# Performance work log

Measured on AMD Instinct MI355X. Metric: run time of the kernel, lower is better.

## Reference

```python
import jax, jax.numpy as jnp
import numpy as np

K = 9          # 3x3 deformable kernel positions
EPS = 1e-5     # BatchNorm eps


def conv3x3(x, w, stride=1):
    # x: [B,C,H,W], w: [O,I,3,3], padding=1
    return jax.lax.conv_general_dilated(
        x, w, (stride, stride), ((1, 1), (1, 1)),
        dimension_numbers=('NCHW', 'OIHW', 'NCHW'))


def _bilinear_sample(img, py, px):
    # img: [C,H,W]; py,px: [K,Ho,Wo] float sample coords (zero outside).
    H, W = img.shape[1], img.shape[2]
    y0 = jnp.floor(py)
    x0 = jnp.floor(px)

    def corner(yc, xc):
        w = (1.0 - jnp.abs(py - yc)) * (1.0 - jnp.abs(px - xc))
        valid = (yc >= 0) & (yc <= H - 1) & (xc >= 0) & (xc <= W - 1)
        yi = jnp.clip(yc, 0, H - 1).astype(jnp.int32)
        xi = jnp.clip(xc, 0, W - 1).astype(jnp.int32)
        v = img[:, yi, xi]                      # [C,K,Ho,Wo]
        return v * (w * valid)[None]

    return (corner(y0, x0) + corner(y0, x0 + 1) +
            corner(y0 + 1, x0) + corner(y0 + 1, x0 + 1))


def deform_conv2d(x, offset, mask, w, stride=1, pad=1):
    # x: [B,Cin,H,W]; offset: [B,2K,Ho,Wo] (y,x interleaved per tap);
    # mask: [B,K,Ho,Wo]; w: [Cout,Cin,3,3]. torchvision DCNv2 semantics.
    B, Cin = x.shape[0], x.shape[1]
    Ho, Wo = offset.shape[2], offset.shape[3]
    Cout = w.shape[0]
    kh, kw = jnp.meshgrid(jnp.arange(3), jnp.arange(3), indexing='ij')
    kh = kh.reshape(K).astype(x.dtype)
    kw = kw.reshape(K).astype(x.dtype)
    base_y = (jnp.arange(Ho) * stride - pad).astype(x.dtype)
    base_x = (jnp.arange(Wo) * stride - pad).astype(x.dtype)
    off = offset.reshape(B, K, 2, Ho, Wo)
    py = base_y[None, None, :, None] + kh[None, :, None, None] + off[:, :, 0]
    px = base_x[None, None, None, :] + kw[None, :, None, None] + off[:, :, 1]
    g = jax.vmap(_bilinear_sample)(x, py, px)     # [B,Cin,K,Ho,Wo]
    g = g * mask[:, None]
    return jnp.einsum('bikhw,oik->bohw', g, w.reshape(Cout, Cin, K))


def batchnorm(x, gamma, beta, mean, var):
    # eval-mode BN over channel dim of [B,C,H,W]
    inv = jax.lax.rsqrt(var + EPS) * gamma
    return x * inv[None, :, None, None] + (beta - mean * inv)[None, :, None, None]


def setup_inputs() -> dict:
    key = jax.random.key(0)
    ks = jax.random.split(key, 20)
    B, Cin, H, W = 16, 64, 64, 64
    C1, C2, NC = 128, 128, 1000
    inp = {
        'x': jax.random.normal(ks[0], (B, Cin, H, W), jnp.float32),
        'conv1_w': jax.random.normal(ks[1], (C1, Cin, 3, 3), jnp.float32) * 0.05,
        'off1_w': jax.random.normal(ks[2], (2 * K, Cin, 3, 3), jnp.float32) * 0.02,
        'mod1_w': jax.random.normal(ks[3], (K, Cin, 3, 3), jnp.float32) * 0.05,
        'bn1_g': jax.random.uniform(ks[4], (C1,), jnp.float32, 0.5, 1.5),
        'bn1_b': jax.random.normal(ks[5], (C1,), jnp.float32) * 0.1,
        'bn1_m': jax.random.normal(ks[6], (C1,), jnp.float32) * 0.1,
        'bn1_v': jax.random.uniform(ks[7], (C1,), jnp.float32, 0.5, 1.5),
        'conv2_w': jax.random.normal(ks[8], (C2, C1, 3, 3), jnp.float32) * 0.05,
        'off2_w': jax.random.normal(ks[9], (2 * K, C1, 3, 3), jnp.float32) * 0.02,
        'mod2_w': jax.random.normal(ks[10], (K, C1, 3, 3), jnp.float32) * 0.05,
        'bn2_g': jax.random.uniform(ks[11], (C2,), jnp.float32, 0.5, 1.5),
        'bn2_b': jax.random.normal(ks[12], (C2,), jnp.float32) * 0.1,
        'bn2_m': jax.random.normal(ks[13], (C2,), jnp.float32) * 0.1,
        'bn2_v': jax.random.uniform(ks[14], (C2,), jnp.float32, 0.5, 1.5),
        'fc_w': jax.random.normal(ks[15], (NC, C2), jnp.float32) * 0.05,
        'fc_b': jnp.zeros((NC,), jnp.float32),
    }
    return inp


def reference(x, conv1_w, off1_w, mod1_w, bn1_g, bn1_b, bn1_m, bn1_v,
              conv2_w, off2_w, mod2_w, bn2_g, bn2_b, bn2_m, bn2_v,
              fc_w, fc_b):
    stride = 1
    # stage 1: deformable conv (offset + sigmoid modulation) + BN + ReLU
    off = conv3x3(x, off1_w, stride)
    mask = jax.nn.sigmoid(conv3x3(x, mod1_w, stride))
    out = deform_conv2d(x, off, mask, conv1_w, stride=stride, pad=1)
    out = jax.nn.relu(batchnorm(out, bn1_g, bn1_b, bn1_m, bn1_v))
    # stage 2: deformable conv + BN (no ReLU before GAP, as in source)
    off = conv3x3(out, off2_w, stride)
    mask = jax.nn.sigmoid(conv3x3(out, mod2_w, stride))
    out = deform_conv2d(out, off, mask, conv2_w, stride=stride, pad=1)
    out = batchnorm(out, bn2_g, bn2_b, bn2_m, bn2_v)
    # global average pool + fc
    out = out.mean(axis=(2, 3))                 # [B, C2]
    return out @ fc_w.T + fc_b
```

## Files before the change

### kernel.cpp

```cpp
#include <hip/hip_runtime.h>

#define TPB 256
typedef unsigned short us;
typedef __attribute__((ext_vector_type(8))) _Float16 f16x8;
typedef __attribute__((ext_vector_type(2))) _Float16 f16x2;
typedef __attribute__((ext_vector_type(4))) float f32x4;

__device__ inline us f2h(float f){ union{ _Float16 h; us u; } x; x.h = (_Float16)f; return x.u; }
__device__ inline f16x2 u2h2(unsigned u){ union{ unsigned v; f16x2 h; } x; x.v = u; return x.h; }
#define MFMA16(a,b,c) __builtin_amdgcn_mfma_f32_16x16x32_f16((a),(b),(c),0,0,0)

__global__ __launch_bounds__(256) void k_transpose_prep(
    const float* __restrict__ x, us* __restrict__ xT,
    const float* __restrict__ cw1, const float* __restrict__ ow1, const float* __restrict__ mw1,
    const float* __restrict__ cw2, const float* __restrict__ ow2, const float* __restrict__ mw2,
    us* __restrict__ d1, us* __restrict__ d2, us* __restrict__ a1, us* __restrict__ a2){
  __shared__ float tile[64][65];
  const int y = blockIdx.x, b = blockIdx.y;
  for (int i = threadIdx.x; i < 4096; i += TPB){
    const int c = i >> 6, xx = i & 63;
    tile[c][xx] = x[b*262144 + c*4096 + y*64 + xx];
  }
  const int e = (blockIdx.y*64 + blockIdx.x)*TPB + threadIdx.x;
  if (e < 73728){
    int k = e/8192, r = e%8192, kb = r/4096, r2 = r%4096;
    int n0 = r2>>9, q = r2&511, l = q>>3, j = q&7;
    int co = n0*16 + (l&15), c = kb*32 + (l>>4)*8 + j;
    d1[e] = f2h(cw1[(co*64 + c)*9 + k]);
  }
  if (e < 147456){
    int k = e/16384, r = e%16384, kb = r/4096, r2 = r%4096;
    int n0 = r2>>9, q = r2&511, l = q>>3, j = q&7;
    int co = n0*16 + (l&15), c = kb*32 + (l>>4)*8 + j;
    d2[e] = f2h(cw2[(co*128 + c)*9 + k]);
  }
  if (e < 18432){
    int k = e/2048, r = e%2048, kb = r/1024, r2 = r%1024;
    int n0 = r2>>9, q = r2&511, l = q>>3, j = q&7;
    int co = n0*16 + (l&15), c = kb*32 + (l>>4)*8 + j;
    float w = (co < 18) ? ow1[(co*64 + c)*9 + k] : (co < 27 ? mw1[((co-18)*64 + c)*9 + k] : 0.f);
    a1[e] = f2h(w);
  }
  if (e < 36864){
    int k = e/4096, r = e%4096, kb = r/1024, r2 = r%1024;
    int n0 = r2>>9, q = r2&511, l = q>>3, j = q&7;
    int co = n0*16 + (l&15), c = kb*32 + (l>>4)*8 + j;
    float w = (co < 18) ? ow2[(co*128 + c)*9 + k] : (co < 27 ? mw2[((co-18)*128 + c)*9 + k] : 0.f);
    a2[e] = f2h(w);
  }
  __syncthreads();
  for (int i = threadIdx.x; i < 4096; i += TPB){
    const int xx = i >> 6, c = i & 63;
    xT[(size_t)(b*4096 + y*64 + xx)*64 + c] = f2h(tile[c][xx]);
  }
}

template<int CIN, int STAGE>
__global__ __launch_bounds__(512, 4) void k_fused(
    const us* __restrict__ inT,
    const us* __restrict__ wb_aux, const us* __restrict__ wb_def,
    const float* __restrict__ bn_g, const float* __restrict__ bn_b,
    const float* __restrict__ bn_m, const float* __restrict__ bn_v,
    us* __restrict__ outT, float* __restrict__ partial){
  constexpr int KB2  = CIN/64;
  constexpr int NC   = 9*KB2;
  constexpr int WE_A = 2*(CIN/32)*512;
  constexpr int WE_D = 8*(CIN/32)*512;

  __shared__ __align__(16) us pool[12672];
  __shared__ uint4 otab[576];
  __shared__ uint2 wtab[576];
  __shared__ float extra[256];

  const int id  = blockIdx.x;
  const int nid = (id & 7)*128 + (id >> 3);
  const int b = nid >> 6, ho = nid & 63;
  const int tid = threadIdx.x;
  const us* __restrict__ inb = inT + (size_t)b*4096*CIN;
  const char* __restrict__ inbc = (const char*)inb;

  if (STAGE == 1 && tid < 128){
    float inv = rsqrtf(bn_v[tid] + 1e-5f)*bn_g[tid];
    extra[tid] = inv; extra[128 + tid] = bn_b[tid] - bn_m[tid]*inv;
  }

  const int lane = tid & 63, lr = lane & 15, lg = lane >> 4;
  const int wv = tid >> 6;
  const int mh = wv & 3, nh = wv >> 2;

  f32x4 aacc = (f32x4){0.f,0.f,0.f,0.f};
  auto load_rows = [&](int kb2, uint4* rq){
    #pragma unroll
    for (int it = 0; it < 4; ++it){
      const int s = it*512 + tid;
      if (s < 1584){
        const int slot = s >> 3, cq = s & 7;
        const int r = slot/66, p = slot - r*66;
        const int y = ho - 1 + r, x = p - 1;
        rq[it] = make_uint4(0u,0u,0u,0u);
        if (y >= 0 && y < 64 && x >= 0 && x < 64)
          rq[it] = *(const uint4*)(inb + (size_t)(y*64 + x)*CIN + kb2*64 + cq*8);
      }
    }
  };
  auto write_rows = [&](const uint4* rq){
    #pragma unroll
    for (int it = 0; it < 4; ++it){
      const int s = it*512 + tid;
      if (s < 1584){
        const int slot = s >> 3, cq = s & 7;
        *(uint4*)(pool + slot*64 + ((cq ^ (slot & 7))*8)) = rq[it];
      }
    }
  };
  auto mfma_aux = [&](int kb2){
    #pragma unroll
    for (int k = 0; k < 9; ++k){
      const int kh = k/3, kw = k - kh*3;
      const int slot = kh*66 + mh*16 + lr + kw;
      #pragma unroll
      for (int kbl = 0; kbl < 2; ++kbl){
        f16x8 a = *(const f16x8*)(pool + slot*64 + (((kbl*4 + lg) ^ (slot & 7))*8));
        f16x8 bf = *(const f16x8*)(wb_aux + (size_t)k*WE_A + (size_t)((kb2*2 + kbl)*2 + nh)*512 + lane*8);
        aacc = MFMA16(a, bf, aacc);
      }
    }
  };
  {
    uint4 rqA[4], rqB[4];
    load_rows(0, rqA);
    write_rows(rqA);
    if constexpr (KB2 == 2) load_rows(1, rqB);
    __syncthreads();
    mfma_aux(0);
    if constexpr (KB2 == 2){
      __syncthreads();
      write_rows(rqB);
      __syncthreads();
      mfma_aux(1);
    }
  }
  __syncthreads();

  float* am = (float*)pool;
  {
    const int co = nh*16 + lr;
    if (co < 27){
      #pragma unroll
      for (int i = 0; i < 4; ++i) am[co*66 + mh*16 + lg*4 + i] = aacc[i];
    }
  }
  __syncthreads();

  for (int sid = tid; sid < 576; sid += 512){
    const int k = sid >> 6, px = sid & 63;
    const int kh = k/3, kw = k - kh*3;
    float oy = am[(2*k)*66 + px];
    float ox = am[(2*k+1)*66 + px];
    float mv = 1.f/(1.f + expf(-am[(18+k)*66 + px]));
    float py  = (float)(ho - 1 + kh) + oy;
    float pxx = (float)(px - 1 + kw) + ox;
    float fyf = floorf(py), fxf = floorf(pxx);
    int y0 = (int)fyf, x0 = (int)fxf;
    float dy = py - fyf, dx = pxx - fxf;
    bool vy0 = (y0 >= 0) && (y0 < 64), vy1 = (y0 >= -1) && (y0 < 63);
    bool vx0 = (x0 >= 0) && (x0 < 64), vx1 = (x0 >= -1) && (x0 < 63);
    int y0c = min(max(y0,0),63), y1c = min(max(y0+1,0),63);
    int x0c = min(max(x0,0),63), x1c = min(max(x0+1,0),63);
    const unsigned str = CIN*2u;
    otab[sid] = make_uint4((unsigned)(y0c*64 + x0c)*str, (unsigned)(y0c*64 + x1c)*str,
                           (unsigned)(y1c*64 + x0c)*str, (unsigned)(y1c*64 + x1c)*str);
    float w00 = (1.f-dy)*(1.f-dx)*mv*((vy0 && vx0) ? 1.f : 0.f);
    float w01 = (1.f-dy)*dx     *mv*((vy0 && vx1) ? 1.f : 0.f);
    float w10 = dy*(1.f-dx)     *mv*((vy1 && vx0) ? 1.f : 0.f);
    float w11 = dy*dx           *mv*((vy1 && vx1) ? 1.f : 0.f);
    wtab[sid] = make_uint2((unsigned)f2h(w00) | ((unsigned)f2h(w01) << 16),
                           (unsigned)f2h(w10) | ((unsigned)f2h(w11) << 16));
  }
  __syncthreads();

  f32x4 acc[4];
  #pragma unroll
  for (int m = 0; m < 4; ++m) acc[m] = (f32x4){0.f,0.f,0.f,0.f};

  const int pxs = tid >> 3, cqs = tid & 7;

  auto load_corners = [&](int i, f16x8* cr){
    const int k = i/KB2, kb2 = i - (i/KB2)*KB2;
    const uint4 o = otab[k*64 + pxs];
    const unsigned c0 = (unsigned)(kb2*64 + cqs*8)*2u;
    cr[0] = *(const f16x8*)(inbc + o.x + c0);
    cr[1] = *(const f16x8*)(inbc + o.y + c0);
    cr[2] = *(const f16x8*)(inbc + o.z + c0);
    cr[3] = *(const f16x8*)(inbc + o.w + c0);
  };
  auto load_B = [&](int i, f16x8* bbp){
    const int k = i/KB2, kb2 = i - (i/KB2)*KB2;
    #pragma unroll
    for (int kbl = 0; kbl < 2; ++kbl)
      bbp[kbl] = *(const f16x8*)(wb_def + (size_t)k*WE_D + (size_t)((kb2*2 + kbl)*8 + wv)*512 + lane*8);
  };
  auto blend_write = [&](int i, const f16x8* cr, us* dst){
    const int k = i/KB2;
    const uint2 wp = wtab[k*64 + pxs];
    const f16x2 wAB = u2h2(wp.x), wCD = u2h2(wp.y);
    const _Float16 wA = wAB[0], wB = wAB[1], wC = wCD[0], wD = wCD[1];
    const f16x8 va = (f16x8){wA,wA,wA,wA,wA,wA,wA,wA};
    const f16x8 vb = (f16x8){wB,wB,wB,wB,wB,wB,wB,wB};
    const f16x8 vc = (f16x8){wC,wC,wC,wC,wC,wC,wC,wC};
    const f16x8 vd = (f16x8){wD,wD,wD,wD,wD,wD,wD,wD};
    f16x8 r = cr[0]*va + cr[1]*vb;
    r = r + cr[2]*vc + cr[3]*vd;
    *(f16x8*)(dst + pxs*64 + ((cqs ^ (pxs & 7))*8)) = r;
  };
  auto mfma_def = [&](int i, const us* src, const f16x8* bbp){
    #pragma unroll
    for (int kbl = 0; kbl < 2; ++kbl){
      #pragma unroll
      for (int mt = 0; mt < 4; ++mt){
        const int row = mt*16 + lr;
        f16x8 a = *(const f16x8*)(src + row*64 + (((kbl*4 + lg) ^ (row & 7))*8));
        acc[mt] = MFMA16(a, bbp[kbl], acc[mt]);
      }
    }
  };

  us* g0 = pool;
  us* g1 = pool + 4096;
  f16x8 crA[4], crB[4], bbA[2], bbB[2];
  load_corners(0, crA); load_B(0, bbA);
  load_corners(1, crB); load_B(1, bbB);
  blend_write(0, crA, g0);
  __syncthreads();
  for (int ii = 0; ii < NC; ii += 2){
    if (ii + 2 < NC) load_corners(ii+2, crA);
    mfma_def(ii, g0, bbA);
    if (ii + 2 < NC) load_B(ii+2, bbA);
    if (ii + 1 < NC) blend_write(ii+1, crB, g1);
    __syncthreads();
    if (ii + 1 < NC){
      if (ii + 3 < NC) load_corners(ii+3, crB);
      mfma_def(ii+1, g1, bbB);
      if (ii + 3 < NC) load_B(ii+3, bbB);
      if (ii + 2 < NC) blend_write(ii+2, crA, g0);
      __syncthreads();
    }
  }

  if (STAGE == 1){
    const size_t rowbase = (size_t)(b*4096 + ho*64)*128;
    const int co = wv*16 + lr;
    const float inv = extra[co], bia = extra[128 + co];
    #pragma unroll
    for (int mt = 0; mt < 4; ++mt){
      const int pxl = mt*16 + lg*4;
      #pragma unroll
      for (int i = 0; i < 4; ++i){
        float v = acc[mt][i]*inv + bia;
        outT[rowbase + (size_t)(pxl + i)*128 + co] = f2h(fmaxf(v, 0.f));
      }
    }
  } else {
    float s = 0.f;
    #pragma unroll
    for (int mt = 0; mt < 4; ++mt)
      s += acc[mt][0] + acc[mt][1] + acc[mt][2] + acc[mt][3];
    s += __shfl_xor(s, 16);
    s += __shfl_xor(s, 32);
    if (lane < 16) extra[wv*16 + lane] = s;
    __syncthreads();
    if (tid < 128) partial[(size_t)(b*64 + ho)*128 + tid] = extra[tid];
  }
}

__global__ __launch_bounds__(256) void k_pool(
    const float* __restrict__ partial,
    const float* __restrict__ g2, const float* __restrict__ b2,
    const float* __restrict__ m2, const float* __restrict__ v2,
    float* __restrict__ pooled){
  const int t = blockIdx.x*TPB + threadIdx.x;
  if (t >= 2048) return;
  const int b = t >> 7, c = t & 127;
  float s = 0.f;
  for (int h = 0; h < 64; ++h) s += partial[(b*64 + h)*128 + c];
  const float inv = rsqrtf(v2[c] + 1e-5f)*g2[c];
  pooled[t] = s*(1.f/4096.f)*inv + (b2[c] - m2[c]*inv);
}

__global__ __launch_bounds__(256) void k_fc(
    const float* __restrict__ pooled, const float* __restrict__ fcw,
    const float* __restrict__ fcb, float* __restrict__ outp){
  const int t = blockIdx.x*TPB + threadIdx.x;
  if (t >= 16000) return;
  const int b = t/1000, n = t - b*1000;
  const float* p = pooled + b*128;
  const float* w = fcw + n*128;
  float s = fcb[n];
  #pragma unroll
  for (int c = 0; c < 128; c += 4){
    const float4 pv = *(const float4*)(p + c);
    const float4 wv = *(const float4*)(w + c);
    s = fmaf(pv.x, wv.x, s); s = fmaf(pv.y, wv.y, s);
    s = fmaf(pv.z, wv.z, s); s = fmaf(pv.w, wv.w, s);
  }
  outp[t] = s;
}

extern "C" void kernel_launch(void* const* d_in, const int* in_sizes, int n_in,
                              void* d_out, int out_size, void* d_ws, size_t ws_size,
                              hipStream_t stream){
  const float* x      = (const float*)d_in[0];
  const float* conv1w = (const float*)d_in[1];
  const float* off1w  = (const float*)d_in[2];
  const float* mod1w  = (const float*)d_in[3];
  const float* bn1g   = (const float*)d_in[4];
  const float* bn1b   = (const float*)d_in[5];
  const float* bn1m   = (const float*)d_in[6];
  const float* bn1v   = (const float*)d_in[7];
  const float* conv2w = (const float*)d_in[8];
  const float* off2w  = (const float*)d_in[9];
  const float* mod2w  = (const float*)d_in[10];
  const float* bn2g   = (const float*)d_in[11];
  const float* bn2b   = (const float*)d_in[12];
  const float* bn2m   = (const float*)d_in[13];
  const float* bn2v   = (const float*)d_in[14];
  const float* fcw    = (const float*)d_in[15];
  const float* fcb    = (const float*)d_in[16];

  char* w = (char*)d_ws;
  us*    xT      = (us*)(w);
  us*    out1T   = (us*)(w + 8388608);
  float* partial = (float*)(w + 25165824);
  float* pooled  = (float*)(w + 25690112);
  us*    wb_d1   = (us*)(w + 25698304);
  us*    wb_d2   = (us*)(w + 25845760);
  us*    wb_a1   = (us*)(w + 26140672);
  us*    wb_a2   = (us*)(w + 26177536);

  k_transpose_prep<<<dim3(64,16), TPB, 0, stream>>>(
      x, xT, conv1w, off1w, mod1w, conv2w, off2w, mod2w,
      wb_d1, wb_d2, wb_a1, wb_a2);

  k_fused<64,1><<<1024, 512, 0, stream>>>(
      xT, wb_a1, wb_d1, bn1g, bn1b, bn1m, bn1v, out1T, nullptr);
  k_fused<128,2><<<1024, 512, 0, stream>>>(
      out1T, wb_a2, wb_d2, nullptr, nullptr, nullptr, nullptr, nullptr, partial);

  k_pool<<<8, TPB, 0, stream>>>(partial, bn2g, bn2b, bn2m, bn2v, pooled);
  k_fc<<<63, TPB, 0, stream>>>(pooled, fcw, fcb, (float*)d_out);
}
```

Baseline: 93.33 us.

## Process two chunks per barrier with quad-buffered LDS in deformable MFMA loop

Restructures the gather-blend/MFMA pipeline so each iteration consumes two chunks and produces the next two into a separate pair of LDS buffers, using four buffers in a ping-pong arrangement. This halves the number of __syncthreads barriers in the main loop and issues more corner loads before the MFMAs, so there is more latency hiding. In exchange, LDS use grows from about 25KB to 32KB per block for the pool, which may reduce occupancy at 512 threads with 4 blocks per CU, and the added in-flight corner registers raise register pressure.

```diff
diff --git a/kernel.cpp b/kernel.cpp
--- a/kernel.cpp
+++ b/kernel.cpp
@@ -64,10 +64,11 @@
     us* __restrict__ outT, float* __restrict__ partial){
   constexpr int KB2  = CIN/64;
   constexpr int NC   = 9*KB2;
+  constexpr int NCP  = NC/2;
   constexpr int WE_A = 2*(CIN/32)*512;
   constexpr int WE_D = 8*(CIN/32)*512;
 
-  __shared__ __align__(16) us pool[12672];
+  __shared__ __align__(16) us pool[16384];
   __shared__ uint4 otab[576];
   __shared__ uint2 wtab[576];
   __shared__ float extra[256];
@@ -225,26 +226,36 @@
     }
   };
 
-  us* g0 = pool;
-  us* g1 = pool + 4096;
+  us* gA0 = pool;
+  us* gA1 = pool + 4096;
+  us* gB0 = pool + 8192;
+  us* gB1 = pool + 12288;
   f16x8 crA[4], crB[4], bbA[2], bbB[2];
   load_corners(0, crA); load_B(0, bbA);
   load_corners(1, crB); load_B(1, bbB);
-  blend_write(0, crA, g0);
-  __syncthreads();
-  for (int ii = 0; ii < NC; ii += 2){
-    if (ii + 2 < NC) load_corners(ii+2, crA);
-    mfma_def(ii, g0, bbA);
-    if (ii + 2 < NC) load_B(ii+2, bbA);
-    if (ii + 1 < NC) blend_write(ii+1, crB, g1);
+  blend_write(0, crA, gA0);
+  blend_write(1, crB, gA1);
+  __syncthreads();
+  for (int pp = 0; pp < NCP; ++pp){
+    const int i = pp*2;
+    us* r0 = (pp & 1) ? gB0 : gA0;
+    us* r1 = (pp & 1) ? gB1 : gA1;
+    us* w0 = (pp & 1) ? gA0 : gB0;
+    us* w1 = (pp & 1) ? gA1 : gB1;
+    const bool m2 = (i + 2 < NC);
+    const bool m3 = (i + 3 < NC);
+    if (m2) load_corners(i+2, crA);
+    if (m3) load_corners(i+3, crB);
+    mfma_def(i, r0, bbA);
+    if (m2) load_B(i+2, bbA);
+    mfma_def(i+1, r1, bbB);
+    if (m3) load_B(i+3, bbB);
+    if (m2) blend_write(i+2, crA, w0);
+    if (m3) blend_write(i+3, crB, w1);
     __syncthreads();
-    if (ii + 1 < NC){
-      if (ii + 3 < NC) load_corners(ii+3, crB);
-      mfma_def(ii+1, g1, bbB);
-      if (ii + 3 < NC) load_B(ii+3, bbB);
-      if (ii + 2 < NC) blend_write(ii+2, crA, g0);
-      __syncthreads();
-    }
+  }
+  if constexpr (NC & 1){
+    mfma_def(NC-1, (NCP & 1) ? gB0 : gA0, bbA);
   }
 
   if (STAGE == 1){
```

Result: no change. 92.86 us (-0.5%).
